# Kernel tuning notes

Hardware: AMD Instinct MI355X
Metric: run time of the kernel (lower is better)

The kernel has to match this reference:

```python
import jax, jax.numpy as jnp
import numpy as np

NUM_TARGETS = 2
N_ITER = 20
REF_MIC = 1          # 1-based reference mic
CONTRAST = 'laplace'
GAMMA = 1.0
PROJ_BACK = 'mdp'
TOL = 1e-5
EPS_R = 1e-10
REG = 1e-6


def contrast_weights(r, func, gamma, eps_r):
    # phi(r) = g'(r) / r for the chosen contrast function
    r = jnp.maximum(r, eps_r)
    if func == 'laplace':
        return 1.0 / (2.0 * r)
    if func == 'gaussian':
        return jnp.ones_like(r)
    if func == 'power':
        return gamma * r ** (gamma - 2.0)
    raise ValueError(func)


def _iva_forward(X):
    M, T, F, _ = X.shape
    K = NUM_TARGETS
    # (M,T,F,2) real/imag -> complex (F,M,T)
    X_c = jnp.transpose(X[..., 0] + 1j * X[..., 1], (2, 0, 1))
    cdtype = X_c.dtype
    eyeM = jnp.eye(M, dtype=cdtype)
    W_hat = jnp.tile(eyeM[None], (F, 1, 1))
    W_hat = W_hat.at[:, K:, K:].set(-jnp.eye(M - K, dtype=cdtype))
    # input covariance (constant over iterations): (F,M,M)
    C = jnp.einsum('fmt,fnt->fmn', X_c, X_c.conj()) / T
    reg_eye = REG * eyeM  # broadcasts over F / (K,F)
    eps = jnp.finfo(jnp.float32).eps
    done = jnp.array(False)

    for _ in range(N_ITER):
        W_old = W_hat
        # current target estimates: (F,K,T)
        Y = jnp.einsum('fkm,fmt->fkt', W_hat[:, :K, :], X_c)
        r = jnp.sqrt(jnp.maximum((jnp.abs(Y) ** 2).sum(axis=0), EPS_R))  # (K,T)
        w_t = contrast_weights(r, CONTRAST, GAMMA, EPS_R).astype(cdtype)
        # weighted covariances: (K,F,M,M)
        V = jnp.einsum('kt,fmt,fnt->kfmn', w_t, X_c, X_c.conj()) / T
        V_reg = V + reg_eye

        Wn = W_hat
        for k in range(K):
            temp = Wn @ V_reg[k]                              # (F,M,M)
            e_k = jnp.zeros((F, M), dtype=cdtype).at[:, k].set(1.0)
            w_vec = jnp.linalg.solve(temp, e_k[..., None])[..., 0]  # (F,M)
            denom = jnp.sqrt(
                jnp.einsum('fm,fmn,fn->f', w_vec.conj(), V_reg[k], w_vec).real + EPS_R
            )
            Wn = Wn.at[:, k, :].set((w_vec / denom[:, None]).conj())
        # background block: J = solve(tmp[:, :, :K], tmp[:, :, K:])^H
        tmp = Wn[:, :K, :] @ C                                # (F,K,M)
        J = jnp.conj(jnp.swapaxes(jnp.linalg.solve(tmp[:, :, :K], tmp[:, :, K:]), 1, 2))
        Wn = Wn.at[:, K:, :K].set(J)

        rel = jnp.linalg.norm(Wn - W_old) / jnp.maximum(jnp.linalg.norm(W_old), eps)
        W_hat = jnp.where(done, W_old, Wn)  # freeze once converged (mimics break)
        done = done | (rel < TOL)

    W = W_hat[:, :K, :]
    Y = jnp.einsum('fkm,fmt->fkt', W, X_c)  # (F,K,T)
    if REF_MIC is not None and 0 < REF_MIC <= M:
        if PROJ_BACK == 'mdp':
            A = jnp.linalg.pinv(W)               # (F,M,K)
            scale = A[:, REF_MIC - 1, :]         # (F,K)
            Y = scale[:, :, None] * Y
        elif PROJ_BACK == 'scale_constraint':
            Wp = jnp.linalg.pinv(W)
            d = jnp.max(jnp.abs(Wp), axis=1)     # (F,K)
            Y = d[:, :, None].astype(cdtype) * Y
    Y_out = jnp.transpose(Y, (1, 2, 0))          # (K,T,F)
    return jnp.stack([Y_out.real, Y_out.imag], axis=-1)


def setup_inputs() -> dict:
    key = jax.random.key(0)
    X = jax.random.normal(key, (8, 2048, 513, 2), dtype=jnp.float32)
    return {"X": X}


def reference(X):
    return _iva_forward(X)
```

## Files before the change

kernel.cpp:

```cpp
#include <hip/hip_runtime.h>

#define F_ 513
#define M_ 8
#define T_ 2048
#define K_ 2
#define NITER 20
#define REGC 1e-6
#define EPSR 1e-10
#define TOLC 1e-5
#define NG 256
#define TS 4
#define UPB ((F_ + 3) / 4)

typedef double2 cd;
__device__ __forceinline__ cd cmk(double r, double i){ cd z; z.x=r; z.y=i; return z; }
__device__ __forceinline__ cd cadd(cd a, cd b){ return cmk(a.x+b.x, a.y+b.y); }
__device__ __forceinline__ cd csub(cd a, cd b){ return cmk(a.x-b.x, a.y-b.y); }
__device__ __forceinline__ cd cmul(cd a, cd b){ return cmk(a.x*b.x - a.y*b.y, a.x*b.y + a.y*b.x); }
__device__ __forceinline__ cd cconj(cd a){ return cmk(a.x, -a.y); }
__device__ __forceinline__ cd cdiv(cd a, cd b){
  double d = b.x*b.x + b.y*b.y;
  return cmk((a.x*b.x + a.y*b.y)/d, (a.y*b.x - a.x*b.y)/d);
}
__device__ __forceinline__ double cabs2(cd a){ return a.x*a.x + a.y*a.y; }
__device__ __forceinline__ cd shflc(cd v, int l){
  cd r; r.x = __shfl(v.x, l, 64); r.y = __shfl(v.y, l, 64); return r;
}
__device__ __forceinline__ cd sel8(const cd x[8], int idx){
  cd r = x[0];
  #pragma unroll
  for (int q=1;q<8;++q) if (idx==q) r = x[q];
  return r;
}

__global__ __launch_bounds__(256) void pack_kernel(const float2* __restrict__ Xin, float2* __restrict__ Xc){
  __shared__ float tr[64][65];
  __shared__ float ti[64][65];
  int f0 = blockIdx.x*64, t0 = blockIdx.y*64, m = blockIdx.z;
  for (int i = threadIdx.x; i < 64*64; i += 256){
    int tl = i >> 6, fl = i & 63;
    int f = f0 + fl;
    float2 v; v.x = 0.f; v.y = 0.f;
    if (f < F_) v = Xin[((size_t)m*T_ + (t0 + tl))*F_ + f];
    tr[tl][fl] = v.x; ti[tl][fl] = v.y;
  }
  __syncthreads();
  for (int i = threadIdx.x; i < 64*32; i += 256){
    int fl = i >> 5, tl2 = i & 31;
    int f = f0 + fl;
    if (f < F_){
      int t = 2*tl2;
      float4 v;
      v.x = tr[t][fl];   v.y = ti[t][fl];
      v.z = tr[t+1][fl]; v.w = ti[t+1][fl];
      *(float4*)&Xc[((size_t)f*8 + m)*T_ + t0 + t] = v;
    }
  }
}

__global__ __launch_bounds__(256) void winit_kernel(float2* __restrict__ W){
  int idx = blockIdx.x*256 + threadIdx.x;
  if (idx >= F_*64) return;
  int l = idx & 63; int i = l>>3, j = l&7;
  float v = (i==j) ? (i < K_ ? 1.f : -1.f) : 0.f;
  float2 o; o.x = v; o.y = 0.f;
  W[idx] = o;
}

template<int MODE>
__global__ __launch_bounds__(512, 8) void cov_kernel(const float2* __restrict__ Xc, const float2* __restrict__ wts2,
                                                     cd* __restrict__ outP, const int* __restrict__ flags){
  if (MODE == 1 && *(volatile const int*)flags) return;
  __shared__ float2 xs[8][514];
  __shared__ float2 wsm2[512];
  int f = blockIdx.x, s = blockIdx.y;
  int tid = threadIdx.x;
  int w = tid >> 6, lane = tid & 63;
  int m = lane >> 3, n = lane & 7;
  #pragma unroll
  for (int r=0; r<4; ++r){
    int idx = tid + r*512;
    int mm = idx >> 8, q = idx & 255;
    float4 v = ((const float4*)(Xc + ((size_t)f*8 + mm)*T_ + s*512))[q];
    *(float4*)&xs[mm][q*2] = v;
  }
  if (MODE == 1) wsm2[tid] = wts2[s*512 + tid];
  __syncthreads();
  const float2* xm = xs[m];
  const float2* xn = xs[n];
  int tbase = w*64;
  float a0r=0.f, a0i=0.f, a1r=0.f, a1i=0.f;
  #pragma unroll 8
  for (int tt=0; tt<64; tt+=2){
    float4 av = *(const float4*)&xm[tbase+tt];
    float4 bv = *(const float4*)&xn[tbase+tt];
    float zr0 = fmaf(av.x, bv.x, av.y*bv.y);
    float zi0 = fmaf(av.y, bv.x, -av.x*bv.y);
    float zr1 = fmaf(av.z, bv.z, av.w*bv.w);
    float zi1 = fmaf(av.w, bv.z, -av.z*bv.w);
    if (MODE == 0){
      a0r += zr0 + zr1; a0i += zi0 + zi1;
    } else {
      float4 wv = *(const float4*)&wsm2[tbase+tt];
      a0r = fmaf(wv.x, zr0, a0r); a0i = fmaf(wv.x, zi0, a0i);
      a1r = fmaf(wv.y, zr0, a1r); a1i = fmaf(wv.y, zi0, a1i);
      a0r = fmaf(wv.z, zr1, a0r); a0i = fmaf(wv.z, zi1, a0i);
      a1r = fmaf(wv.w, zr1, a1r); a1i = fmaf(wv.w, zi1, a1i);
    }
  }
  __syncthreads();
  float* wred = (float*)&xs[0][0];
  wred[0*512 + w*64 + lane] = a0r;
  wred[1*512 + w*64 + lane] = a0i;
  if (MODE == 1){
    wred[2*512 + w*64 + lane] = a1r;
    wred[3*512 + w*64 + lane] = a1i;
  }
  __syncthreads();
  const double inv = 1.0/(double)T_;
  int nk = (MODE == 0) ? 1 : 2;
  if (tid < nk*64){
    int k = tid >> 6, l = tid & 63;
    float rr = 0.f, ii = 0.f;
    #pragma unroll
    for (int ww=0; ww<8; ++ww){
      rr += wred[(k*2+0)*512 + ww*64 + l];
      ii += wred[(k*2+1)*512 + ww*64 + l];
    }
    cd o = cmk((double)rr*inv, (double)ii*inv);
    if (MODE == 0) outP[((size_t)f*TS + s)*64 + l] = o;
    else           outP[(((size_t)k*F_ + f)*TS + s)*64 + l] = o;
  }
}

__global__ __launch_bounds__(256) void yr_kernel(const float2* __restrict__ Xc, const float2* __restrict__ Wg,
                                                 float* __restrict__ part, const int* __restrict__ flags){
  if (*(volatile const int*)flags) return;
  int g = blockIdx.y;
  int t = blockIdx.x*256 + threadIdx.x;
  float acc0 = 0.f, acc1 = 0.f;
  for (int f = g; f < F_; f += NG){
    const float2* Wf = Wg + (size_t)f*64;
    float2 y0; y0.x=0; y0.y=0;
    float2 y1; y1.x=0; y1.y=0;
    #pragma unroll
    for (int m=0;m<8;++m){
      float2 xv = Xc[((size_t)f*8 + m)*T_ + t];
      float2 w0 = Wf[m];
      float2 w1 = Wf[8+m];
      y0.x = fmaf(w0.x,xv.x,fmaf(-w0.y,xv.y,y0.x)); y0.y = fmaf(w0.x,xv.y,fmaf(w0.y,xv.x,y0.y));
      y1.x = fmaf(w1.x,xv.x,fmaf(-w1.y,xv.y,y1.x)); y1.y = fmaf(w1.x,xv.y,fmaf(w1.y,xv.x,y1.y));
    }
    acc0 += y0.x*y0.x + y0.y*y0.y;
    acc1 += y1.x*y1.x + y1.y*y1.y;
  }
  part[((size_t)g*2+0)*T_ + t] = acc0;
  part[((size_t)g*2+1)*T_ + t] = acc1;
}

__global__ __launch_bounds__(256) void rw_kernel(const float* __restrict__ part, float* __restrict__ wts2f,
                                                 const int* __restrict__ flags){
  if (*(volatile const int*)flags) return;
  int v = blockIdx.x*256 + threadIdx.x;
  int k = v >> 11, t = v & (T_-1);
  double s = 0;
  for (int g=0; g<NG; ++g) s += (double)part[((size_t)g*2+k)*T_ + t];
  wts2f[2*t + k] = (float)(0.5 / sqrt(fmax(s, EPSR)));
}

__global__ __launch_bounds__(256) void update_kernel(const cd* __restrict__ Vp, const cd* __restrict__ Cp,
                                                     float2* __restrict__ Wg,
                                                     double* __restrict__ dsum, double* __restrict__ osum,
                                                     int* __restrict__ flags){
  if (*(volatile const int*)flags) return;
  int lane = threadIdx.x & 63;
  int w = threadIdx.x >> 6;
  int f = blockIdx.x*4 + w;
  int i = lane >> 3, j = lane & 7;
  double ds = 0.0, os = 0.0;
  if (f < F_){
    float2 wf = Wg[(size_t)f*64 + lane];
    cd Wn = cmk(wf.x, wf.y);
    cd Wold = Wn;
    cd x[8];
    #pragma unroll
    for (int k=0; k<K_; ++k){
      cd Vr = cmk(0,0);
      #pragma unroll
      for (int s2=0; s2<TS; ++s2)
        Vr = cadd(Vr, Vp[(((size_t)k*F_ + f)*TS + s2)*64 + lane]);
      if (i == j) Vr.x += REGC;
      cd temp = cmk(0,0);
      #pragma unroll
      for (int q=0;q<8;++q) temp = cadd(temp, cmul(shflc(Wn, i*8+q), shflc(Vr, q*8+j)));
      cd b = cmk(i==k ? 1.0 : 0.0, 0.0);
      for (int p=0; p<8; ++p){
        double pv = (j==p && i>=p) ? cabs2(temp) : -1.0;
        int pidx = i;
        for (int off=32; off; off>>=1){
          double ov = __shfl_xor(pv, off, 64);
          int oi = __shfl_xor(pidx, off, 64);
          if (ov > pv){ pv = ov; pidx = oi; }
        }
        cd tp = shflc(temp, pidx*8 + j);
        cd tq = shflc(temp, p*8 + j);
        cd bp_ = shflc(b, pidx*8 + j);
        cd bq_ = shflc(b, p*8 + j);
        if (i == p){ temp = tp; b = bp_; }
        else if (i == pidx){ temp = tq; b = bq_; }
        cd tip = shflc(temp, i*8 + p);
        cd tpp = shflc(temp, p*8 + p);
        cd tpj = shflc(temp, p*8 + j);
        cd bpr = shflc(b, p*8 + j);
        cd fac = cdiv(tip, tpp);
        if (i > p){ temp = csub(temp, cmul(fac, tpj)); b = csub(b, cmul(fac, bpr)); }
      }
      #pragma unroll
      for (int p=7; p>=0; --p){
        cd s = shflc(b, p*8);
        #pragma unroll
        for (int q=p+1; q<8; ++q){
          cd tpq = shflc(temp, p*8 + q);
          s = csub(s, cmul(tpq, x[q]));
        }
        x[p] = cdiv(s, shflc(temp, p*8 + p));
      }
      cd xi = sel8(x, i), xj = sel8(x, j);
      cd z = cmul(cconj(xi), Vr);
      double dl = z.x*xj.x - z.y*xj.y;
      for (int off=32; off; off>>=1) dl += __shfl_xor(dl, off, 64);
      double denom = sqrt(dl + EPSR);
      if (i == k){ Wn = cmk(xj.x/denom, -xj.y/denom); }
    }
    cd Cc = cmk(0,0);
    #pragma unroll
    for (int s2=0; s2<TS; ++s2)
      Cc = cadd(Cc, Cp[((size_t)f*TS + s2)*64 + lane]);
    cd tmp = cmk(0,0);
    #pragma unroll
    for (int q=0;q<8;++q) tmp = cadd(tmp, cmul(shflc(Wn, i*8+q), shflc(Cc, q*8+j)));
    cd A = shflc(tmp, 0), B = shflc(tmp, 1), C2 = shflc(tmp, 8), D = shflc(tmp, 9);
    cd det = csub(cmul(A,D), cmul(B,C2));
    cd t0 = shflc(tmp, i);
    cd t1 = shflc(tmp, 8 + i);
    cd Z0 = cdiv(csub(cmul(D,t0), cmul(B,t1)), det);
    cd Z1 = cdiv(csub(cmul(A,t1), cmul(C2,t0)), det);
    if (i >= K_ && j < K_){
      cd Z = (j==0) ? Z0 : Z1;
      Wn = cconj(Z);
    }
    ds = cabs2(csub(Wn, Wold));
    os = cabs2(Wold);
    for (int off=32; off; off>>=1){
      ds += __shfl_xor(ds, off, 64);
      os += __shfl_xor(os, off, 64);
    }
    float2 wo; wo.x = (float)Wn.x; wo.y = (float)Wn.y;
    Wg[(size_t)f*64 + lane] = wo;
  }
  __shared__ double sd[4], so[4];
  __shared__ int lastFlag;
  if (lane == 0){ sd[w] = ds; so[w] = os; }
  __syncthreads();
  if (threadIdx.x == 0){
    dsum[blockIdx.x] = sd[0]+sd[1]+sd[2]+sd[3];
    osum[blockIdx.x] = so[0]+so[1]+so[2]+so[3];
  }
  __threadfence();
  if (threadIdx.x == 0){
    int tk = atomicAdd(&flags[1], 1);
    lastFlag = (tk == UPB-1) ? 1 : 0;
  }
  __syncthreads();
  if (lastFlag && threadIdx.x < 64){
    __threadfence();
    double d=0, o=0;
    for (int idx=lane; idx<UPB; idx+=64){
      d += ((volatile double*)dsum)[idx];
      o += ((volatile double*)osum)[idx];
    }
    for (int off=32; off; off>>=1){ d += __shfl_xor(d, off, 64); o += __shfl_xor(o, off, 64); }
    if (lane == 0){
      flags[1] = 0;
      double rel = sqrt(d) / fmax(sqrt(o), 1.1920928955078125e-7);
      if (rel < TOLC) flags[0] = 1;
    }
  }
}

__global__ __launch_bounds__(256) void scale_kernel(const float2* __restrict__ Wg, float2* __restrict__ scale){
  int f = blockIdx.x*256 + threadIdx.x;
  if (f >= F_) return;
  cd w0[8], w1[8];
  #pragma unroll
  for (int m=0;m<8;++m){
    float2 a = Wg[(size_t)f*64 + m];     w0[m] = cmk(a.x, a.y);
    float2 b = Wg[(size_t)f*64 + 8 + m]; w1[m] = cmk(b.x, b.y);
  }
  cd G00 = cmk(0,0), G01 = cmk(0,0), G11 = cmk(0,0);
  #pragma unroll
  for (int m=0;m<8;++m){
    G00 = cadd(G00, cmul(w0[m], cconj(w0[m])));
    G01 = cadd(G01, cmul(w0[m], cconj(w1[m])));
    G11 = cadd(G11, cmul(w1[m], cconj(w1[m])));
  }
  cd G10 = cconj(G01);
  cd det = csub(cmul(G00,G11), cmul(G01,G10));
  cd I00 = cdiv(G11, det), I01 = cdiv(cmk(-G01.x,-G01.y), det);
  cd I10 = cdiv(cmk(-G10.x,-G10.y), det), I11 = cdiv(G00, det);
  cd c0 = cconj(w0[0]), c1 = cconj(w1[0]);
  cd s0 = cadd(cmul(c0, I00), cmul(c1, I10));
  cd s1 = cadd(cmul(c0, I01), cmul(c1, I11));
  float2 o0; o0.x=(float)s0.x; o0.y=(float)s0.y;
  float2 o1; o1.x=(float)s1.x; o1.y=(float)s1.y;
  scale[(size_t)f*2 + 0] = o0;
  scale[(size_t)f*2 + 1] = o1;
}

__global__ __launch_bounds__(256) void out_kernel(const float2* __restrict__ Xc, const float2* __restrict__ Wg,
                                                  const float2* __restrict__ scale, float2* __restrict__ out){
  __shared__ float re0[32][65], im0[32][65], re1[32][65], im1[32][65];
  int f0 = blockIdx.x*32, t0 = blockIdx.y*64;
  int lane = threadIdx.x & 63, w = threadIdx.x >> 6;
  for (int fl = w; fl < 32; fl += 4){
    int f = f0 + fl;
    if (f < F_){
      const float2* Wf = Wg + (size_t)f*64;
      int t = t0 + lane;
      float2 y0; y0.x=0; y0.y=0;
      float2 y1; y1.x=0; y1.y=0;
      #pragma unroll
      for (int m=0;m<8;++m){
        float2 xv = Xc[((size_t)f*8 + m)*T_ + t];
        float2 w0 = Wf[m];
        float2 w1 = Wf[8+m];
        y0.x += w0.x*xv.x - w0.y*xv.y; y0.y += w0.x*xv.y + w0.y*xv.x;
        y1.x += w1.x*xv.x - w1.y*xv.y; y1.y += w1.x*xv.y + w1.y*xv.x;
      }
      float2 s0 = scale[(size_t)f*2 + 0];
      float2 s1 = scale[(size_t)f*2 + 1];
      re0[fl][lane] = s0.x*y0.x - s0.y*y0.y; im0[fl][lane] = s0.x*y0.y + s0.y*y0.x;
      re1[fl][lane] = s1.x*y1.x - s1.y*y1.y; im1[fl][lane] = s1.x*y1.y + s1.y*y1.x;
    }
  }
  __syncthreads();
  for (int i = threadIdx.x; i < 32*64; i += 256){
    int tl = i >> 5, fl = i & 31;
    int f = f0 + fl;
    if (f < F_){
      int t = t0 + tl;
      float2 o0; o0.x = re0[fl][tl]; o0.y = im0[fl][tl];
      float2 o1; o1.x = re1[fl][tl]; o1.y = im1[fl][tl];
      out[((size_t)(0*T_ + t))*F_ + f] = o0;
      out[((size_t)(1*T_ + t))*F_ + f] = o1;
    }
  }
}

extern "C" void kernel_launch(void* const* d_in, const int* in_sizes, int n_in,
                              void* d_out, int out_size, void* d_ws, size_t ws_size,
                              hipStream_t stream) {
  const float2* Xin = (const float2*)d_in[0];
  char* ws = (char*)d_ws;
  size_t off = 0;
  auto alloc = [&](size_t bytes) -> void* {
    void* p = ws + off;
    off += (bytes + 255) & ~(size_t)255;
    return p;
  };
  float2* Xc   = (float2*)alloc((size_t)F_*M_*T_*8);
  cd*     Cp   = (cd*)alloc((size_t)F_*TS*64*16);
  cd*     Vp   = (cd*)alloc((size_t)K_*F_*TS*64*16);
  float2* W    = (float2*)alloc((size_t)F_*64*8);
  float*  part = (float*)alloc((size_t)NG*K_*T_*4);
  float2* wts2 = (float2*)alloc((size_t)T_*8);
  double* dsum = (double*)alloc((size_t)UPB*8);
  double* osum = (double*)alloc((size_t)UPB*8);
  float2* sc   = (float2*)alloc((size_t)F_*K_*8);
  int*    flags= (int*)alloc(256);
  if (off > ws_size) return;

  hipMemsetAsync(flags, 0, 12, stream);

  pack_kernel<<<dim3(9, 32, 8), 256, 0, stream>>>(Xin, Xc);
  winit_kernel<<<(F_*64 + 255)/256, 256, 0, stream>>>(W);
  cov_kernel<0><<<dim3(F_, TS), 512, 0, stream>>>(Xc, nullptr, Cp, flags);

  for (int it=0; it<NITER; ++it){
    yr_kernel<<<dim3(T_/256, NG), 256, 0, stream>>>(Xc, W, part, flags);
    rw_kernel<<<(K_*T_ + 255)/256, 256, 0, stream>>>(part, (float*)wts2, flags);
    cov_kernel<1><<<dim3(F_, TS), 512, 0, stream>>>(Xc, wts2, Vp, flags);
    update_kernel<<<UPB, 256, 0, stream>>>(Vp, Cp, W, dsum, osum, flags);
  }

  scale_kernel<<<(F_ + 255)/256, 256, 0, stream>>>(W, sc);
  out_kernel<<<dim3(17, 32), 256, 0, stream>>>(Xc, W, sc, (float2*)d_out);
}
```

Before: 1.670 ms.

## Fuse IVA iteration loop into one persistent cooperative kernel with grid syncs

Replaces the 80 per-iteration kernel launches (yr, rw, cov, update) with a single cooperative persistent kernel of 1024 blocks that uses grid.sync between phases. Each block owns fixed (f, time-segment) tiles, and the last block to finish a frequency's weighted covariance solves the demixing update for it right away, chained by per-frequency atomic tickets. The goal is to remove launch overhead and to cut the work the launches spread across many blocks. The cost is three grid-wide barriers per iteration, per-frequency atomics, a different covariance tiling, and a fallback multi-kernel path if the cooperative launch is unavailable. The pack kernel tile height is also halved.

```diff
diff --git a/kernel.cpp b/kernel.cpp
--- a/kernel.cpp
+++ b/kernel.cpp
@@ -1,4 +1,7 @@
 #include <hip/hip_runtime.h>
+#include <hip/hip_cooperative_groups.h>
+
+namespace cg = cooperative_groups;
 
 #define F_ 513
 #define M_ 8
@@ -11,6 +14,7 @@
 #define NG 256
 #define TS 4
 #define UPB ((F_ + 3) / 4)
+#define NBC 1024
 
 typedef double2 cd;
 __device__ __forceinline__ cd cmk(double r, double i){ cd z; z.x=r; z.y=i; return z; }
@@ -33,11 +37,259 @@
   return r;
 }
 
+__device__ __forceinline__ void solve_f(int f, int lane,
+    const cd* __restrict__ Vp, const cd* __restrict__ Cp,
+    float2* __restrict__ Wg, double* __restrict__ dsum, double* __restrict__ osum)
+{
+  int i = lane >> 3, j = lane & 7;
+  float2 wf = Wg[(size_t)f*64 + lane];
+  cd Wn = cmk(wf.x, wf.y);
+  cd Wold = Wn;
+  cd x[8];
+  #pragma unroll
+  for (int k=0; k<K_; ++k){
+    cd Vr = cmk(0,0);
+    #pragma unroll
+    for (int s2=0; s2<TS; ++s2)
+      Vr = cadd(Vr, Vp[(((size_t)k*F_ + f)*TS + s2)*64 + lane]);
+    if (i == j) Vr.x += REGC;
+    cd temp = cmk(0,0);
+    #pragma unroll
+    for (int q=0;q<8;++q) temp = cadd(temp, cmul(shflc(Wn, i*8+q), shflc(Vr, q*8+j)));
+    cd b = cmk(i==k ? 1.0 : 0.0, 0.0);
+    for (int p=0; p<8; ++p){
+      double pv = (j==p && i>=p) ? cabs2(temp) : -1.0;
+      int pidx = i;
+      for (int off=32; off; off>>=1){
+        double ov = __shfl_xor(pv, off, 64);
+        int oi = __shfl_xor(pidx, off, 64);
+        if (ov > pv){ pv = ov; pidx = oi; }
+      }
+      cd tp = shflc(temp, pidx*8 + j);
+      cd tq = shflc(temp, p*8 + j);
+      cd bp_ = shflc(b, pidx*8 + j);
+      cd bq_ = shflc(b, p*8 + j);
+      if (i == p){ temp = tp; b = bp_; }
+      else if (i == pidx){ temp = tq; b = bq_; }
+      cd tip = shflc(temp, i*8 + p);
+      cd tpp = shflc(temp, p*8 + p);
+      cd tpj = shflc(temp, p*8 + j);
+      cd bpr = shflc(b, p*8 + j);
+      cd fac = cdiv(tip, tpp);
+      if (i > p){ temp = csub(temp, cmul(fac, tpj)); b = csub(b, cmul(fac, bpr)); }
+    }
+    #pragma unroll
+    for (int p=7; p>=0; --p){
+      cd s = shflc(b, p*8);
+      #pragma unroll
+      for (int q=p+1; q<8; ++q){
+        cd tpq = shflc(temp, p*8 + q);
+        s = csub(s, cmul(tpq, x[q]));
+      }
+      x[p] = cdiv(s, shflc(temp, p*8 + p));
+    }
+    cd xi = sel8(x, i), xj = sel8(x, j);
+    cd z = cmul(cconj(xi), Vr);
+    double dl = z.x*xj.x - z.y*xj.y;
+    for (int off=32; off; off>>=1) dl += __shfl_xor(dl, off, 64);
+    double denom = sqrt(dl + EPSR);
+    if (i == k){ Wn = cmk(xj.x/denom, -xj.y/denom); }
+  }
+  cd Cc = cmk(0,0);
+  #pragma unroll
+  for (int s2=0; s2<TS; ++s2)
+    Cc = cadd(Cc, Cp[((size_t)f*TS + s2)*64 + lane]);
+  cd tmp = cmk(0,0);
+  #pragma unroll
+  for (int q=0;q<8;++q) tmp = cadd(tmp, cmul(shflc(Wn, i*8+q), shflc(Cc, q*8+j)));
+  cd A = shflc(tmp, 0), B = shflc(tmp, 1), C2 = shflc(tmp, 8), D = shflc(tmp, 9);
+  cd det = csub(cmul(A,D), cmul(B,C2));
+  cd t0 = shflc(tmp, i);
+  cd t1 = shflc(tmp, 8 + i);
+  cd Z0 = cdiv(csub(cmul(D,t0), cmul(B,t1)), det);
+  cd Z1 = cdiv(csub(cmul(A,t1), cmul(C2,t0)), det);
+  if (i >= K_ && j < K_){
+    cd Z = (j==0) ? Z0 : Z1;
+    Wn = cconj(Z);
+  }
+  double ds = cabs2(csub(Wn, Wold));
+  double os = cabs2(Wold);
+  for (int off=32; off; off>>=1){
+    ds += __shfl_xor(ds, off, 64);
+    os += __shfl_xor(os, off, 64);
+  }
+  float2 wo; wo.x = (float)Wn.x; wo.y = (float)Wn.y;
+  Wg[(size_t)f*64 + lane] = wo;
+  if (lane == 0){ dsum[f] = ds; osum[f] = os; }
+}
+
+__global__ __launch_bounds__(256, 4) void iva_loop_kernel(
+    const float2* __restrict__ Xc, const cd* __restrict__ Cp,
+    float2* __restrict__ Wg, float2* __restrict__ partF,
+    float2* __restrict__ wts2, cd* __restrict__ Vp,
+    double* __restrict__ dsum, double* __restrict__ osum,
+    int* __restrict__ flags, int* __restrict__ tickf)
+{
+  cg::grid_group grid = cg::this_grid();
+  __shared__ float2 xbuf[8][132];
+  __shared__ float wredV[4][4][64];
+  __shared__ double wredR[4][64][2];
+  __shared__ int solvN;
+  __shared__ int solvF[4];
+  int bid = blockIdx.x;
+  int tid = threadIdx.x;
+  int w = tid >> 6, lane = tid & 63;
+  int m = lane >> 3, n = lane & 7;
+  int tiles[3];
+  tiles[0] = 2*bid; tiles[1] = 2*bid+1; tiles[2] = (bid < 4) ? 2048 + bid : -1;
+
+  for (int it = 0; it < NITER; ++it){
+    #pragma unroll 1
+    for (int sel = 0; sel < 3; ++sel){
+      int tile = tiles[sel];
+      if (tile < 0) continue;
+      int f = tile >> 2, s = tile & 3;
+      const float2* Wf = Wg + (size_t)f*64;
+      float2 w0f[8], w1f[8];
+      #pragma unroll
+      for (int mm=0; mm<8; ++mm){ w0f[mm] = Wf[mm]; w1f[mm] = Wf[8+mm]; }
+      int t = s*512 + tid*2;
+      float2 y00={0,0}, y01={0,0}, y10={0,0}, y11={0,0};
+      #pragma unroll
+      for (int mm=0; mm<8; ++mm){
+        float4 xv = *(const float4*)&Xc[((size_t)f*8+mm)*T_ + t];
+        float2 a = w0f[mm], b2 = w1f[mm];
+        y00.x = fmaf(a.x,xv.x,fmaf(-a.y,xv.y,y00.x)); y00.y = fmaf(a.x,xv.y,fmaf(a.y,xv.x,y00.y));
+        y10.x = fmaf(b2.x,xv.x,fmaf(-b2.y,xv.y,y10.x)); y10.y = fmaf(b2.x,xv.y,fmaf(b2.y,xv.x,y10.y));
+        y01.x = fmaf(a.x,xv.z,fmaf(-a.y,xv.w,y01.x)); y01.y = fmaf(a.x,xv.w,fmaf(a.y,xv.z,y01.y));
+        y11.x = fmaf(b2.x,xv.z,fmaf(-b2.y,xv.w,y11.x)); y11.y = fmaf(b2.x,xv.w,fmaf(b2.y,xv.z,y11.y));
+      }
+      float4 pr;
+      pr.x = fmaf(y00.x,y00.x,y00.y*y00.y);
+      pr.y = fmaf(y10.x,y10.x,y10.y*y10.y);
+      pr.z = fmaf(y01.x,y01.x,y01.y*y01.y);
+      pr.w = fmaf(y11.x,y11.x,y11.y*y11.y);
+      *(float4*)&partF[(size_t)f*T_ + t] = pr;
+    }
+    __threadfence();
+    grid.sync();
+    if (bid < 32){
+      int t = bid*64 + lane;
+      double s0=0, s1=0;
+      for (int f=w; f<F_; f+=4){
+        float2 p = partF[(size_t)f*T_ + t];
+        s0 += (double)p.x; s1 += (double)p.y;
+      }
+      wredR[w][lane][0]=s0; wredR[w][lane][1]=s1;
+      __syncthreads();
+      if (tid < 64){
+        double a=0,b2=0;
+        #pragma unroll
+        for (int ww=0; ww<4; ++ww){ a += wredR[ww][tid][0]; b2 += wredR[ww][tid][1]; }
+        wts2[bid*64+tid] = make_float2((float)(0.5/sqrt(fmax(a,EPSR))),
+                                       (float)(0.5/sqrt(fmax(b2,EPSR))));
+      }
+      __threadfence();
+    }
+    grid.sync();
+    if (tid == 0) solvN = 0;
+    __syncthreads();
+    #pragma unroll 1
+    for (int sel = 0; sel < 3; ++sel){
+      int tile = tiles[sel];
+      if (tile < 0) continue;
+      int f = tile >> 2, s = tile & 3;
+      float a0r=0.f, a0i=0.f, a1r=0.f, a1i=0.f;
+      #pragma unroll 1
+      for (int c=0; c<4; ++c){
+        __syncthreads();
+        #pragma unroll
+        for (int r=0; r<2; ++r){
+          int idx = tid + r*256;
+          int mm = idx >> 6, q = idx & 63;
+          float4 v = *(const float4*)&Xc[((size_t)f*8+mm)*T_ + s*512 + c*128 + q*2];
+          *(float4*)&xbuf[mm][q*2] = v;
+        }
+        __syncthreads();
+        const float2* xm = xbuf[m];
+        const float2* xn = xbuf[n];
+        int tb = w*32;
+        #pragma unroll
+        for (int tt=0; tt<32; tt+=2){
+          float4 av = *(const float4*)&xm[tb+tt];
+          float4 bv = *(const float4*)&xn[tb+tt];
+          float zr0 = fmaf(av.x,bv.x, av.y*bv.y);
+          float zi0 = fmaf(av.y,bv.x,-av.x*bv.y);
+          float zr1 = fmaf(av.z,bv.z, av.w*bv.w);
+          float zi1 = fmaf(av.w,bv.z,-av.z*bv.w);
+          float4 wv = *(const float4*)&wts2[s*512 + c*128 + tb + tt];
+          a0r = fmaf(wv.x, zr0, a0r); a0i = fmaf(wv.x, zi0, a0i);
+          a1r = fmaf(wv.y, zr0, a1r); a1i = fmaf(wv.y, zi0, a1i);
+          a0r = fmaf(wv.z, zr1, a0r); a0i = fmaf(wv.z, zi1, a0i);
+          a1r = fmaf(wv.w, zr1, a1r); a1i = fmaf(wv.w, zi1, a1i);
+        }
+      }
+      __syncthreads();
+      wredV[0][w][lane]=a0r; wredV[1][w][lane]=a0i;
+      wredV[2][w][lane]=a1r; wredV[3][w][lane]=a1i;
+      __syncthreads();
+      if (tid < 128){
+        int k = tid >> 6, l = tid & 63;
+        float rr=0.f, ii=0.f;
+        #pragma unroll
+        for (int ww=0; ww<4; ++ww){ rr += wredV[2*k][ww][l]; ii += wredV[2*k+1][ww][l]; }
+        const double inv = 1.0/(double)T_;
+        Vp[(((size_t)k*F_+f)*TS + s)*64 + l] = cmk((double)rr*inv, (double)ii*inv);
+      }
+      __threadfence();
+      __syncthreads();
+      if (tid == 0){
+        int tk = atomicAdd(&tickf[f], 1);
+        if (tk == TS-1){
+          tickf[f] = 0;
+          solvF[solvN] = f;
+          solvN = solvN + 1;
+        }
+      }
+    }
+    __syncthreads();
+    int ns = solvN;
+    if (w < ns){
+      int f = solvF[w];
+      solve_f(f, lane, Vp, Cp, Wg, dsum, osum);
+      int lastw = 0;
+      if (lane == 0){
+        __threadfence();
+        lastw = (atomicAdd(&flags[1], 1) == F_-1) ? 1 : 0;
+      }
+      lastw = __shfl(lastw, 0, 64);
+      if (lastw){
+        __threadfence();
+        double d=0, o=0;
+        for (int idx=lane; idx<F_; idx+=64){
+          d += ((volatile double*)dsum)[idx];
+          o += ((volatile double*)osum)[idx];
+        }
+        for (int off=32; off; off>>=1){ d += __shfl_xor(d, off, 64); o += __shfl_xor(o, off, 64); }
+        if (lane == 0){
+          flags[1] = 0;
+          double rel = sqrt(d) / fmax(sqrt(o), 1.1920928955078125e-7);
+          if (rel < TOLC) flags[0] = 1;
+        }
+      }
+    }
+    __threadfence();
+    grid.sync();
+    if (*(volatile int*)&flags[0]) break;
+  }
+}
+
+
 __global__ __launch_bounds__(256) void pack_kernel(const float2* __restrict__ Xin, float2* __restrict__ Xc){
-  __shared__ float tr[64][65];
-  __shared__ float ti[64][65];
-  int f0 = blockIdx.x*64, t0 = blockIdx.y*64, m = blockIdx.z;
-  for (int i = threadIdx.x; i < 64*64; i += 256){
+  __shared__ float tr[32][65];
+  __shared__ float ti[32][65];
+  int f0 = blockIdx.x*64, t0 = blockIdx.y*32, m = blockIdx.z;
+  for (int i = threadIdx.x; i < 32*64; i += 256){
     int tl = i >> 6, fl = i & 63;
     int f = f0 + fl;
     float2 v; v.x = 0.f; v.y = 0.f;
@@ -45,8 +297,8 @@
     tr[tl][fl] = v.x; ti[tl][fl] = v.y;
   }
   __syncthreads();
-  for (int i = threadIdx.x; i < 64*32; i += 256){
-    int fl = i >> 5, tl2 = i & 31;
+  for (int i = threadIdx.x; i < 64*16; i += 256){
+    int fl = i >> 4, tl2 = i & 15;
     int f = f0 + fl;
     if (f < F_){
       int t = 2*tl2;
@@ -67,12 +319,9 @@
   W[idx] = o;
 }
 
-template<int MODE>
-__global__ __launch_bounds__(512, 8) void cov_kernel(const float2* __restrict__ Xc, const float2* __restrict__ wts2,
-                                                     cd* __restrict__ outP, const int* __restrict__ flags){
-  if (MODE == 1 && *(volatile const int*)flags) return;
+__global__ __launch_bounds__(512) void cov0_kernel(const float2* __restrict__ Xc, cd* __restrict__ Cp){
   __shared__ float2 xs[8][514];
-  __shared__ float2 wsm2[512];
+  __shared__ double wred[2][8][64];
   int f = blockIdx.x, s = blockIdx.y;
   int tid = threadIdx.x;
   int w = tid >> 6, lane = tid & 63;
@@ -84,57 +333,31 @@
     float4 v = ((const float4*)(Xc + ((size_t)f*8 + mm)*T_ + s*512))[q];
     *(float4*)&xs[mm][q*2] = v;
   }
-  if (MODE == 1) wsm2[tid] = wts2[s*512 + tid];
   __syncthreads();
   const float2* xm = xs[m];
   const float2* xn = xs[n];
   int tbase = w*64;
-  float a0r=0.f, a0i=0.f, a1r=0.f, a1i=0.f;
+  float ar=0.f, ai=0.f;
   #pragma unroll 8
   for (int tt=0; tt<64; tt+=2){
     float4 av = *(const float4*)&xm[tbase+tt];
     float4 bv = *(const float4*)&xn[tbase+tt];
-    float zr0 = fmaf(av.x, bv.x, av.y*bv.y);
-    float zi0 = fmaf(av.y, bv.x, -av.x*bv.y);
-    float zr1 = fmaf(av.z, bv.z, av.w*bv.w);
-    float zi1 = fmaf(av.w, bv.z, -av.z*bv.w);
-    if (MODE == 0){
-      a0r += zr0 + zr1; a0i += zi0 + zi1;
-    } else {
-      float4 wv = *(const float4*)&wsm2[tbase+tt];
-      a0r = fmaf(wv.x, zr0, a0r); a0i = fmaf(wv.x, zi0, a0i);
-      a1r = fmaf(wv.y, zr0, a1r); a1i = fmaf(wv.y, zi0, a1i);
-      a0r = fmaf(wv.z, zr1, a0r); a0i = fmaf(wv.z, zi1, a0i);
-      a1r = fmaf(wv.w, zr1, a1r); a1i = fmaf(wv.w, zi1, a1i);
-    }
-  }
-  __syncthreads();
-  float* wred = (float*)&xs[0][0];
-  wred[0*512 + w*64 + lane] = a0r;
-  wred[1*512 + w*64 + lane] = a0i;
-  if (MODE == 1){
-    wred[2*512 + w*64 + lane] = a1r;
-    wred[3*512 + w*64 + lane] = a1i;
-  }
-  __syncthreads();
-  const double inv = 1.0/(double)T_;
-  int nk = (MODE == 0) ? 1 : 2;
-  if (tid < nk*64){
-    int k = tid >> 6, l = tid & 63;
-    float rr = 0.f, ii = 0.f;
+    ar += fmaf(av.x, bv.x, av.y*bv.y) + fmaf(av.z, bv.z, av.w*bv.w);
+    ai += fmaf(av.y, bv.x, -av.x*bv.y) + fmaf(av.w, bv.z, -av.z*bv.w);
+  }
+  wred[0][w][lane] = ar; wred[1][w][lane] = ai;
+  __syncthreads();
+  if (tid < 64){
+    double sr=0, si=0;
     #pragma unroll
-    for (int ww=0; ww<8; ++ww){
-      rr += wred[(k*2+0)*512 + ww*64 + l];
-      ii += wred[(k*2+1)*512 + ww*64 + l];
-    }
-    cd o = cmk((double)rr*inv, (double)ii*inv);
-    if (MODE == 0) outP[((size_t)f*TS + s)*64 + l] = o;
-    else           outP[(((size_t)k*F_ + f)*TS + s)*64 + l] = o;
-  }
-}
-
-__global__ __launch_bounds__(256) void yr_kernel(const float2* __restrict__ Xc, const float2* __restrict__ Wg,
-                                                 float* __restrict__ part, const int* __restrict__ flags){
+    for (int ww=0; ww<8; ++ww){ sr += wred[0][ww][tid]; si += wred[1][ww][tid]; }
+    const double inv = 1.0/(double)T_;
+    Cp[((size_t)f*TS + s)*64 + tid] = cmk(sr*inv, si*inv);
+  }
+}
+
+__global__ __launch_bounds__(256) void yrF_kernel(const float2* __restrict__ Xc, const float2* __restrict__ Wg,
+                                                  float* __restrict__ part, const int* __restrict__ flags){
   if (*(volatile const int*)flags) return;
   int g = blockIdx.y;
   int t = blockIdx.x*256 + threadIdx.x;
@@ -158,8 +381,8 @@
   part[((size_t)g*2+1)*T_ + t] = acc1;
 }
 
-__global__ __launch_bounds__(256) void rw_kernel(const float* __restrict__ part, float* __restrict__ wts2f,
-                                                 const int* __restrict__ flags){
+__global__ __launch_bounds__(256) void rwF_kernel(const float* __restrict__ part, float* __restrict__ wts2f,
+                                                  const int* __restrict__ flags){
   if (*(volatile const int*)flags) return;
   int v = blockIdx.x*256 + threadIdx.x;
   int k = v >> 11, t = v & (T_-1);
@@ -168,105 +391,74 @@
   wts2f[2*t + k] = (float)(0.5 / sqrt(fmax(s, EPSR)));
 }
 
-__global__ __launch_bounds__(256) void update_kernel(const cd* __restrict__ Vp, const cd* __restrict__ Cp,
-                                                     float2* __restrict__ Wg,
-                                                     double* __restrict__ dsum, double* __restrict__ osum,
-                                                     int* __restrict__ flags){
+__global__ __launch_bounds__(512, 8) void covF_kernel(const float2* __restrict__ Xc, const float2* __restrict__ wts2,
+                                                      cd* __restrict__ outP, const int* __restrict__ flags){
+  if (*(volatile const int*)flags) return;
+  __shared__ float2 xs[8][514];
+  __shared__ float2 wsm2[512];
+  int f = blockIdx.x, s = blockIdx.y;
+  int tid = threadIdx.x;
+  int w = tid >> 6, lane = tid & 63;
+  int m = lane >> 3, n = lane & 7;
+  #pragma unroll
+  for (int r=0; r<4; ++r){
+    int idx = tid + r*512;
+    int mm = idx >> 8, q = idx & 255;
+    float4 v = ((const float4*)(Xc + ((size_t)f*8 + mm)*T_ + s*512))[q];
+    *(float4*)&xs[mm][q*2] = v;
+  }
+  wsm2[tid] = wts2[s*512 + tid];
+  __syncthreads();
+  const float2* xm = xs[m];
+  const float2* xn = xs[n];
+  int tbase = w*64;
+  float a0r=0.f, a0i=0.f, a1r=0.f, a1i=0.f;
+  #pragma unroll 8
+  for (int tt=0; tt<64; tt+=2){
+    float4 av = *(const float4*)&xm[tbase+tt];
+    float4 bv = *(const float4*)&xn[tbase+tt];
+    float zr0 = fmaf(av.x, bv.x, av.y*bv.y);
+    float zi0 = fmaf(av.y, bv.x, -av.x*bv.y);
+    float zr1 = fmaf(av.z, bv.z, av.w*bv.w);
+    float zi1 = fmaf(av.w, bv.z, -av.z*bv.w);
+    float4 wv = *(const float4*)&wsm2[tbase+tt];
+    a0r = fmaf(wv.x, zr0, a0r); a0i = fmaf(wv.x, zi0, a0i);
+    a1r = fmaf(wv.y, zr0, a1r); a1i = fmaf(wv.y, zi0, a1i);
+    a0r = fmaf(wv.z, zr1, a0r); a0i = fmaf(wv.z, zi1, a0i);
+    a1r = fmaf(wv.w, zr1, a1r); a1i = fmaf(wv.w, zi1, a1i);
+  }
+  __syncthreads();
+  float* wred = (float*)&xs[0][0];
+  wred[0*512 + w*64 + lane] = a0r;
+  wred[1*512 + w*64 + lane] = a0i;
+  wred[2*512 + w*64 + lane] = a1r;
+  wred[3*512 + w*64 + lane] = a1i;
+  __syncthreads();
+  const double inv = 1.0/(double)T_;
+  if (tid < 128){
+    int k = tid >> 6, l = tid & 63;
+    float rr = 0.f, ii = 0.f;
+    #pragma unroll
+    for (int ww=0; ww<8; ++ww){
+      rr += wred[(k*2+0)*512 + ww*64 + l];
+      ii += wred[(k*2+1)*512 + ww*64 + l];
+    }
+    outP[(((size_t)k*F_ + f)*TS + s)*64 + l] = cmk((double)rr*inv, (double)ii*inv);
+  }
+}
+
+__global__ __launch_bounds__(256) void updF_kernel(const cd* __restrict__ Vp, const cd* __restrict__ Cp,
+                                                   float2* __restrict__ Wg,
+                                                   double* __restrict__ dsum, double* __restrict__ osum,
+                                                   int* __restrict__ flags){
   if (*(volatile const int*)flags) return;
   int lane = threadIdx.x & 63;
   int w = threadIdx.x >> 6;
   int f = blockIdx.x*4 + w;
-  int i = lane >> 3, j = lane & 7;
-  double ds = 0.0, os = 0.0;
-  if (f < F_){
-    float2 wf = Wg[(size_t)f*64 + lane];
-    cd Wn = cmk(wf.x, wf.y);
-    cd Wold = Wn;
-    cd x[8];
-    #pragma unroll
-    for (int k=0; k<K_; ++k){
-      cd Vr = cmk(0,0);
-      #pragma unroll
-      for (int s2=0; s2<TS; ++s2)
-        Vr = cadd(Vr, Vp[(((size_t)k*F_ + f)*TS + s2)*64 + lane]);
-      if (i == j) Vr.x += REGC;
-      cd temp = cmk(0,0);
-      #pragma unroll
-      for (int q=0;q<8;++q) temp = cadd(temp, cmul(shflc(Wn, i*8+q), shflc(Vr, q*8+j)));
-      cd b = cmk(i==k ? 1.0 : 0.0, 0.0);
-      for (int p=0; p<8; ++p){
-        double pv = (j==p && i>=p) ? cabs2(temp) : -1.0;
-        int pidx = i;
-        for (int off=32; off; off>>=1){
-          double ov = __shfl_xor(pv, off, 64);
-          int oi = __shfl_xor(pidx, off, 64);
-          if (ov > pv){ pv = ov; pidx = oi; }
-        }
-        cd tp = shflc(temp, pidx*8 + j);
-        cd tq = shflc(temp, p*8 + j);
-        cd bp_ = shflc(b, pidx*8 + j);
-        cd bq_ = shflc(b, p*8 + j);
-        if (i == p){ temp = tp; b = bp_; }
-        else if (i == pidx){ temp = tq; b = bq_; }
-        cd tip = shflc(temp, i*8 + p);
-        cd tpp = shflc(temp, p*8 + p);
-        cd tpj = shflc(temp, p*8 + j);
-        cd bpr = shflc(b, p*8 + j);
-        cd fac = cdiv(tip, tpp);
-        if (i > p){ temp = csub(temp, cmul(fac, tpj)); b = csub(b, cmul(fac, bpr)); }
-      }
-      #pragma unroll
-      for (int p=7; p>=0; --p){
-        cd s = shflc(b, p*8);
-        #pragma unroll
-        for (int q=p+1; q<8; ++q){
-          cd tpq = shflc(temp, p*8 + q);
-          s = csub(s, cmul(tpq, x[q]));
-        }
-        x[p] = cdiv(s, shflc(temp, p*8 + p));
-      }
-      cd xi = sel8(x, i), xj = sel8(x, j);
-      cd z = cmul(cconj(xi), Vr);
-      double dl = z.x*xj.x - z.y*xj.y;
-      for (int off=32; off; off>>=1) dl += __shfl_xor(dl, off, 64);
-      double denom = sqrt(dl + EPSR);
-      if (i == k){ Wn = cmk(xj.x/denom, -xj.y/denom); }
-    }
-    cd Cc = cmk(0,0);
-    #pragma unroll
-    for (int s2=0; s2<TS; ++s2)
-      Cc = cadd(Cc, Cp[((size_t)f*TS + s2)*64 + lane]);
-    cd tmp = cmk(0,0);
-    #pragma unroll
-    for (int q=0;q<8;++q) tmp = cadd(tmp, cmul(shflc(Wn, i*8+q), shflc(Cc, q*8+j)));
-    cd A = shflc(tmp, 0), B = shflc(tmp, 1), C2 = shflc(tmp, 8), D = shflc(tmp, 9);
-    cd det = csub(cmul(A,D), cmul(B,C2));
-    cd t0 = shflc(tmp, i);
-    cd t1 = shflc(tmp, 8 + i);
-    cd Z0 = cdiv(csub(cmul(D,t0), cmul(B,t1)), det);
-    cd Z1 = cdiv(csub(cmul(A,t1), cmul(C2,t0)), det);
-    if (i >= K_ && j < K_){
-      cd Z = (j==0) ? Z0 : Z1;
-      Wn = cconj(Z);
-    }
-    ds = cabs2(csub(Wn, Wold));
-    os = cabs2(Wold);
-    for (int off=32; off; off>>=1){
-      ds += __shfl_xor(ds, off, 64);
-      os += __shfl_xor(os, off, 64);
-    }
-    float2 wo; wo.x = (float)Wn.x; wo.y = (float)Wn.y;
-    Wg[(size_t)f*64 + lane] = wo;
-  }
-  __shared__ double sd[4], so[4];
+  if (f < F_) solve_f(f, lane, Vp, Cp, Wg, dsum, osum);
   __shared__ int lastFlag;
-  if (lane == 0){ sd[w] = ds; so[w] = os; }
-  __syncthreads();
-  if (threadIdx.x == 0){
-    dsum[blockIdx.x] = sd[0]+sd[1]+sd[2]+sd[3];
-    osum[blockIdx.x] = so[0]+so[1]+so[2]+so[3];
-  }
   __threadfence();
+  __syncthreads();
   if (threadIdx.x == 0){
     int tk = atomicAdd(&flags[1], 1);
     lastFlag = (tk == UPB-1) ? 1 : 0;
@@ -275,7 +467,7 @@
   if (lastFlag && threadIdx.x < 64){
     __threadfence();
     double d=0, o=0;
-    for (int idx=lane; idx<UPB; idx+=64){
+    for (int idx=lane; idx<F_; idx+=64){
       d += ((volatile double*)dsum)[idx];
       o += ((volatile double*)osum)[idx];
     }
@@ -368,29 +560,46 @@
     off += (bytes + 255) & ~(size_t)255;
     return p;
   };
-  float2* Xc   = (float2*)alloc((size_t)F_*M_*T_*8);
-  cd*     Cp   = (cd*)alloc((size_t)F_*TS*64*16);
-  cd*     Vp   = (cd*)alloc((size_t)K_*F_*TS*64*16);
-  float2* W    = (float2*)alloc((size_t)F_*64*8);
-  float*  part = (float*)alloc((size_t)NG*K_*T_*4);
-  float2* wts2 = (float2*)alloc((size_t)T_*8);
-  double* dsum = (double*)alloc((size_t)UPB*8);
-  double* osum = (double*)alloc((size_t)UPB*8);
-  float2* sc   = (float2*)alloc((size_t)F_*K_*8);
-  int*    flags= (int*)alloc(256);
+  float2* Xc    = (float2*)alloc((size_t)F_*M_*T_*8);
+  cd*     Cp    = (cd*)alloc((size_t)F_*TS*64*16);
+  cd*     Vp    = (cd*)alloc((size_t)K_*F_*TS*64*16);
+  float2* W     = (float2*)alloc((size_t)F_*64*8);
+  float2* partF = (float2*)alloc((size_t)F_*T_*8);
+  float*  partG = (float*)alloc((size_t)NG*K_*T_*4);
+  float2* wts2  = (float2*)alloc((size_t)T_*8);
+  double* dsum  = (double*)alloc((size_t)F_*8);
+  double* osum  = (double*)alloc((size_t)F_*8);
+  float2* sc    = (float2*)alloc((size_t)F_*K_*8);
+  int*    ibuf  = (int*)alloc(4096);
   if (off > ws_size) return;
-
-  hipMemsetAsync(flags, 0, 12, stream);
-
-  pack_kernel<<<dim3(9, 32, 8), 256, 0, stream>>>(Xin, Xc);
+  int* flags = ibuf;
+  int* tickf = ibuf + 256;
+
+  hipMemsetAsync(ibuf, 0, 4096, stream);
+
+  pack_kernel<<<dim3(9, 64, 8), 256, 0, stream>>>(Xin, Xc);
   winit_kernel<<<(F_*64 + 255)/256, 256, 0, stream>>>(W);
-  cov_kernel<0><<<dim3(F_, TS), 512, 0, stream>>>(Xc, nullptr, Cp, flags);
-
-  for (int it=0; it<NITER; ++it){
-    yr_kernel<<<dim3(T_/256, NG), 256, 0, stream>>>(Xc, W, part, flags);
-    rw_kernel<<<(K_*T_ + 255)/256, 256, 0, stream>>>(part, (float*)wts2, flags);
-    cov_kernel<1><<<dim3(F_, TS), 512, 0, stream>>>(Xc, wts2, Vp, flags);
-    update_kernel<<<UPB, 256, 0, stream>>>(Vp, Cp, W, dsum, osum, flags);
+  cov0_kernel<<<dim3(F_, TS), 512, 0, stream>>>(Xc, Cp);
+
+  bool coop_ok = false;
+  int mb = 0;
+  hipError_t e0 = hipOccupancyMaxActiveBlocksPerMultiprocessor(
+      &mb, reinterpret_cast<const void*>(iva_loop_kernel), 256, 0);
+  if (e0 == hipSuccess && mb >= 4){
+    void* args[] = { (void*)&Xc, (void*)&Cp, (void*)&W, (void*)&partF, (void*)&wts2,
+                     (void*)&Vp, (void*)&dsum, (void*)&osum, (void*)&flags, (void*)&tickf };
+    hipError_t e1 = hipLaunchCooperativeKernel(
+        reinterpret_cast<const void*>(iva_loop_kernel),
+        dim3(NBC), dim3(256), args, 0, stream);
+    if (e1 == hipSuccess) coop_ok = true;
+  }
+  if (!coop_ok){
+    for (int it=0; it<NITER; ++it){
+      yrF_kernel<<<dim3(T_/256, NG), 256, 0, stream>>>(Xc, W, partG, flags);
+      rwF_kernel<<<(K_*T_ + 255)/256, 256, 0, stream>>>(partG, (float*)wts2, flags);
+      covF_kernel<<<dim3(F_, TS), 512, 0, stream>>>(Xc, wts2, Vp, flags);
+      updF_kernel<<<UPB, 256, 0, stream>>>(Vp, Cp, W, dsum, osum, flags);
+    }
   }
 
   scale_kernel<<<(F_ + 255)/256, 256, 0, stream>>>(W, sc);
```

Result: no change. 1.701 ms (+1.8%).
